# Kernel tuning notes

Measured on AMD Instinct MI355X. Metric: run time of the kernel, lower is better.

The kernel has to match this reference:

```python
import jax, jax.numpy as jnp
import numpy as np

N_NODES = 50000
N_EDGES = 640000
N_GRAPHS = 64
IN_DIM, HID, OUT_DIM = 128, 256, 4


def gcn_conv(x, src, dst, W, b, n_nodes):
    """PyG GCNConv: linear transform, then sym-normalized aggregation with self-loops."""
    h = x @ W  # [N, out]
    deg = jnp.zeros((n_nodes,), h.dtype).at[dst].add(1.0) + 1.0  # +1 self-loop
    dinv = jax.lax.rsqrt(deg)  # deg >= 1 always
    norm = dinv[src] * dinv[dst]  # [E]
    msg = h[src] * norm[:, None]  # [E, out]  gather + scale
    agg = jax.ops.segment_sum(msg, dst, num_segments=n_nodes)  # scatter-add
    agg = agg + h * (dinv * dinv)[:, None]  # self-loop contribution
    return agg + b


def global_mean_pool(x, batch, num_graphs):
    s = jax.ops.segment_sum(x, batch, num_segments=num_graphs)
    cnt = jax.ops.segment_sum(jnp.ones((x.shape[0],), x.dtype), batch, num_segments=num_graphs)
    return s / jnp.clip(cnt, 1.0)[:, None]


def setup_inputs() -> dict:
    key = jax.random.key(0)
    ks = jax.random.split(key, 8)
    x = jax.random.normal(ks[0], (N_NODES, IN_DIM), jnp.float32)
    src = jax.random.randint(ks[1], (N_EDGES,), 0, N_NODES, jnp.int64 if jax.config.jax_enable_x64 else jnp.int32)
    dst = jax.random.randint(ks[2], (N_EDGES,), 0, N_NODES, src.dtype)
    batch = jnp.sort(jax.random.randint(ks[3], (N_NODES,), 0, N_GRAPHS, src.dtype))
    W1 = jax.random.normal(ks[4], (IN_DIM, HID), jnp.float32) * (1.0 / np.sqrt(IN_DIM))
    b1 = jnp.zeros((HID,), jnp.float32)
    W2 = jax.random.normal(ks[5], (HID, HID // 2), jnp.float32) * (1.0 / np.sqrt(HID))
    b2 = jnp.zeros((HID // 2,), jnp.float32)
    Wfc = jax.random.normal(ks[6], (HID // 2, OUT_DIM), jnp.float32) * (1.0 / np.sqrt(HID // 2))
    bfc = jnp.zeros((OUT_DIM,), jnp.float32)
    return {"x": x, "src": src, "dst": dst, "batch": batch,
            "W1": W1, "b1": b1, "W2": W2, "b2": b2, "Wfc": Wfc, "bfc": bfc}


def reference(x, src, dst, batch, W1, b1, W2, b2, Wfc, bfc):
    n = x.shape[0]
    h = jax.nn.relu(gcn_conv(x, src, dst, W1, b1, n))   # dropout is identity at inference
    h = jax.nn.relu(gcn_conv(h, src, dst, W2, b2, n))
    g = global_mean_pool(h, batch, N_GRAPHS)            # [G, HID//2]
    return g @ Wfc + bfc                                # [G, OUT_DIM]
```

## Files before the change

### kernel.cpp

```cpp
#include <hip/hip_runtime.h>


constexpr int IN_DIM  = 128;
constexpr int HID     = 256;
constexpr int HID2    = 128;
constexpr int OUT_DIM = 4;
constexpr int NGRAPH  = 64;

typedef __attribute__((ext_vector_type(8))) short bf16x8;
typedef __attribute__((ext_vector_type(4))) float f32x4;

__device__ __forceinline__ short f2bf(float f) {
    union { float f; unsigned u; } v; v.f = f;
    unsigned r = v.u + 0x7fff + ((v.u >> 16) & 1);
    return (short)(r >> 16);
}
__device__ __forceinline__ float bf2f(short s) {
    union { unsigned u; float f; } v; v.u = ((unsigned)(unsigned short)s) << 16;
    return v.f;
}


__global__ void wprep_all_kernel(const float* __restrict__ W1, short* __restrict__ W1th,
                                 short* __restrict__ W1tl,
                                 const float* __restrict__ W2, short* __restrict__ W2th,
                                 short* __restrict__ W2tl,
                                 int* __restrict__ count, float* __restrict__ pool, int N) {
    int i = blockIdx.x * blockDim.x + threadIdx.x;
    if (i < IN_DIM * HID) {
        int k = i / HID, n = i % HID;
        float w = W1[i];
        short h = f2bf(w);
        W1th[n * IN_DIM + k] = h;
        W1tl[n * IN_DIM + k] = f2bf(w - bf2f(h));
    }
    if (i < HID * HID2) {
        int k = i / HID2, n = i % HID2;
        float w = W2[i];
        short h = f2bf(w);
        W2th[n * HID + k] = h;
        W2tl[n * HID + k] = f2bf(w - bf2f(h));
    }
    if (i < N) count[i] = 0;
    if (i < NGRAPH * HID2) pool[i] = 0.f;
}


__global__ void hist_kernel(const int* __restrict__ dst, int* __restrict__ count,
                            ushort* __restrict__ rank, int E) {
    int i = blockIdx.x * blockDim.x + threadIdx.x;
    if (i < E) rank[i] = (ushort)atomicAdd(&count[dst[i]], 1);
}

__global__ void scan1_kernel(const int* __restrict__ count, int* __restrict__ bsums, int N) {
    __shared__ int s[256];
    int t = threadIdx.x, i = blockIdx.x * 256 + t;
    int v = (i < N) ? count[i] : 0;
    s[t] = v; __syncthreads();
    for (int o = 1; o < 256; o <<= 1) {
        int x = (t >= o) ? s[t - o] : 0;
        __syncthreads(); s[t] += x; __syncthreads();
    }
    if (t == 255) bsums[blockIdx.x] = s[255];
}

__global__ void scan3_kernel(const int* __restrict__ count, const int* __restrict__ bsums,
                             int* __restrict__ rowptr, float* __restrict__ dinv,
                             int N, int E, int nb) {
    __shared__ int sb[256];
    __shared__ int s[256];
    int t = threadIdx.x, i = blockIdx.x * 256 + t;
    int bv = (t < nb) ? bsums[t] : 0;
    sb[t] = bv; __syncthreads();
    for (int o = 1; o < 256; o <<= 1) {
        int x = (t >= o) ? sb[t - o] : 0;
        __syncthreads(); sb[t] += x; __syncthreads();
    }
    int myex = (blockIdx.x == 0) ? 0 : sb[blockIdx.x - 1];
    int v = (i < N) ? count[i] : 0;
    s[t] = v; __syncthreads();
    for (int o = 1; o < 256; o <<= 1) {
        int x = (t >= o) ? s[t - o] : 0;
        __syncthreads(); s[t] += x; __syncthreads();
    }
    if (i < N) {
        rowptr[i] = myex + s[t] - v;
        dinv[i] = rsqrtf((float)v + 1.0f);
        if (i == 0) rowptr[N] = E;
    }
}

__global__ void scatter_scale_kernel(const int* __restrict__ src, const int* __restrict__ dst,
                                     const ushort* __restrict__ rank,
                                     const int* __restrict__ rowptr, ushort* __restrict__ csr,
                                     const float* __restrict__ x, const float* __restrict__ dinv,
                                     ushort* __restrict__ xb, int E, int total2) {
    int i = blockIdx.x * blockDim.x + threadIdx.x;
    if (i < E) {
        int p = rowptr[dst[i]] + (int)rank[i];
        csr[p] = (ushort)src[i];
    }
    if (i < total2) {
        float d = dinv[i >> 6];
        float2 v = ((const float2*)x)[i];
        ushort2 o;
        o.x = (ushort)f2bf(v.x * d);
        o.y = (ushort)f2bf(v.y * d);
        ((ushort2*)xb)[i] = o;
    }
}


__launch_bounds__(256, 2)
__global__ void mlp_fused_kernel(const short* __restrict__ A,
                                 const short* __restrict__ W1h, const short* __restrict__ W1l,
                                 const float* __restrict__ b1,
                                 const short* __restrict__ W2h, const short* __restrict__ W2l,
                                 const float* __restrict__ dinv,
                                 short* __restrict__ Cb, int M) {
    __shared__ __align__(16) short L[12288 + 6144];
    short* A1 = L;
    short* A0 = L + 12288;
    __shared__ float dinv_s[48];

    const int tid  = threadIdx.x;
    const int w    = tid >> 6;
    const int lane = tid & 63;
    const int l15  = lane & 15;
    const int kq8  = (lane >> 4) * 8;
    const int row0 = blockIdx.x * 48;

    const short* w1hp = W1h + (size_t)(w * 64 + l15) * IN_DIM + kq8;
    const short* w1lp = W1l + (size_t)(w * 64 + l15) * IN_DIM + kq8;
    bf16x8 wh1[4][4], wl1[4][4];
#pragma unroll
    for (int ks = 0; ks < 4; ++ks)
#pragma unroll
        for (int n = 0; n < 4; ++n) {
            wh1[ks][n] = *(const bf16x8*)(w1hp + (size_t)(n * 16) * IN_DIM + ks * 32);
            wl1[ks][n] = *(const bf16x8*)(w1lp + (size_t)(n * 16) * IN_DIM + ks * 32);
        }

    {
        bf16x8 stg[3];
#pragma unroll
        for (int j = 0; j < 3; ++j) {
            int s = w * 3 + j;
            int m = s >> 2, ks = s & 3;
            int rr = row0 + m * 16 + l15; if (rr >= M) rr = M - 1;
            stg[j] = *(const bf16x8*)(A + (size_t)rr * IN_DIM + ks * 32 + kq8);
        }
#pragma unroll
        for (int j = 0; j < 3; ++j)
            *(bf16x8*)&A0[(w * 3 + j) * 512 + lane * 8] = stg[j];
    }
    if (tid < 48) { int r = row0 + tid; dinv_s[tid] = dinv[r < M ? r : M - 1]; }
    __syncthreads();

    f32x4 acc1[3][4];
#pragma unroll
    for (int m = 0; m < 3; ++m)
#pragma unroll
        for (int n = 0; n < 4; ++n) acc1[m][n] = f32x4{0.f, 0.f, 0.f, 0.f};

#pragma unroll
    for (int ks = 0; ks < 4; ++ks) {
        bf16x8 af[3];
#pragma unroll
        for (int m = 0; m < 3; ++m) af[m] = *(const bf16x8*)&A0[(m * 4 + ks) * 512 + lane * 8];
#pragma unroll
        for (int m = 0; m < 3; ++m)
#pragma unroll
            for (int n = 0; n < 4; ++n) {
                acc1[m][n] = __builtin_amdgcn_mfma_f32_16x16x32_bf16(af[m], wh1[ks][n], acc1[m][n], 0, 0, 0);
                acc1[m][n] = __builtin_amdgcn_mfma_f32_16x16x32_bf16(af[m], wl1[ks][n], acc1[m][n], 0, 0, 0);
            }
    }

#pragma unroll
    for (int n = 0; n < 4; ++n) {
        int c  = w * 64 + n * 16 + l15;
        float bv = b1[c];
        int kst = c >> 5;
        int q  = (c >> 3) & 3;
        int e  = c & 7;
#pragma unroll
        for (int m = 0; m < 3; ++m)
#pragma unroll
            for (int r4 = 0; r4 < 4; ++r4) {
                int rl = (lane >> 4) * 4 + r4;
                int d  = rl + 16 * q;
                float v = fmaxf(acc1[m][n][r4] + bv, 0.f);
                A1[(m * 8 + kst) * 512 + d * 8 + e] = f2bf(v);
            }
    }

    const short* w2hp = W2h + (size_t)(w * 32 + l15) * HID + kq8;
    const short* w2lp = W2l + (size_t)(w * 32 + l15) * HID + kq8;
    bf16x8 wh2[8][2], wl2[8][2];
#pragma unroll
    for (int ks = 0; ks < 8; ++ks)
#pragma unroll
        for (int n = 0; n < 2; ++n) {
            wh2[ks][n] = *(const bf16x8*)(w2hp + (size_t)(n * 16) * HID + ks * 32);
            wl2[ks][n] = *(const bf16x8*)(w2lp + (size_t)(n * 16) * HID + ks * 32);
        }
    __syncthreads();

    f32x4 acc2[3][2];
#pragma unroll
    for (int m = 0; m < 3; ++m)
#pragma unroll
        for (int n = 0; n < 2; ++n) acc2[m][n] = f32x4{0.f, 0.f, 0.f, 0.f};

#pragma unroll
    for (int ks = 0; ks < 8; ++ks) {
        bf16x8 af[3];
#pragma unroll
        for (int m = 0; m < 3; ++m) af[m] = *(const bf16x8*)&A1[(m * 8 + ks) * 512 + lane * 8];
#pragma unroll
        for (int m = 0; m < 3; ++m)
#pragma unroll
            for (int n = 0; n < 2; ++n) {
                acc2[m][n] = __builtin_amdgcn_mfma_f32_16x16x32_bf16(af[m], wh2[ks][n], acc2[m][n], 0, 0, 0);
                acc2[m][n] = __builtin_amdgcn_mfma_f32_16x16x32_bf16(af[m], wl2[ks][n], acc2[m][n], 0, 0, 0);
            }
    }
    __syncthreads();

    short* T = A1;
#pragma unroll
    for (int n = 0; n < 2; ++n) {
        int c = w * 32 + n * 16 + l15;
#pragma unroll
        for (int m = 0; m < 3; ++m)
#pragma unroll
            for (int r4 = 0; r4 < 4; ++r4) {
                int r = m * 16 + (lane >> 4) * 4 + r4;
                T[r * 132 + c] = f2bf(acc2[m][n][r4] * dinv_s[r]);
            }
    }
    __syncthreads();
#pragma unroll
    for (int it = 0; it < 3; ++it) {
        int chunk = it * 256 + tid;
        int lr = chunk >> 4;
        int lc = (chunk & 15) * 8;
        int gr = row0 + lr;
        if (gr < M)
            *(bf16x8*)(Cb + (size_t)gr * HID2 + lc) = *(const bf16x8*)&T[lr * 132 + lc];
    }
}


template <bool POOL>
__launch_bounds__(256)
__global__ void agg_group_kernel(const ushort* __restrict__ hb, const float* __restrict__ dinv,
                                 const int* __restrict__ rowptr, const ushort* __restrict__ csr,
                                 const float* __restrict__ bias,
                                 short* __restrict__ oh,
                                 const int* __restrict__ batch, float* __restrict__ pool,
                                 int N) {
    __shared__ float pacc[16][128];
    __shared__ int   sgid[16];

    const int tid  = threadIdx.x;
    const int li   = tid & 15;
    const int nib  = tid >> 4;
    const int node = blockIdx.x * 16 + nib;
    const bool valid = node < N;
    if (!POOL && !valid) return;
    const int cw = valid ? node : N - 1;

    const int lo = rowptr[cw], hi = rowptr[cw + 1];
    const float dd = dinv[cw];

    float a[8];
    {
        bf16x8 sv = *(const bf16x8*)(hb + ((size_t)cw << 7) + (li << 3));
#pragma unroll
        for (int d = 0; d < 8; ++d) a[d] = bf2f(sv[d]);
    }

    const ushort* hsl = hb + (li << 3);

    for (int base = lo; base < hi; base += 16) {
        int cnt = min(16, hi - base);
        int sidx = (int)csr[base + (li < cnt ? li : cnt - 1)];
        bf16x8 p[8], q[8];
#pragma unroll
        for (int u = 0; u < 8; ++u) {
            int s = __shfl(sidx, u < cnt ? u : cnt - 1, 16);
            p[u] = *(const bf16x8*)(hsl + ((size_t)s << 7));
        }
#pragma unroll
        for (int u = 0; u < 8; ++u) {
            int e = 8 + u;
            int s = __shfl(sidx, e < cnt ? e : cnt - 1, 16);
            q[u] = *(const bf16x8*)(hsl + ((size_t)s << 7));
        }
#pragma unroll
        for (int u = 0; u < 8; ++u) {
            bool v = u < cnt;
#pragma unroll
            for (int d = 0; d < 8; ++d) a[d] += v ? bf2f(p[u][d]) : 0.f;
        }
#pragma unroll
        for (int u = 0; u < 8; ++u) {
            bool v = 8 + u < cnt;
#pragma unroll
            for (int d = 0; d < 8; ++d) a[d] += v ? bf2f(q[u][d]) : 0.f;
        }
    }

#pragma unroll
    for (int d = 0; d < 8; ++d) a[d] *= dd;

    if (!POOL) {
        if (valid) {
            bf16x8 o;
#pragma unroll
            for (int d = 0; d < 8; ++d) o[d] = f2bf(a[d]);
            *(bf16x8*)&oh[(size_t)node * 128 + li * 8] = o;
        }
        return;
    }

    {
        float4 b0 = ((const float4*)bias)[li * 2];
        float4 b1 = ((const float4*)bias)[li * 2 + 1];
        a[0] = fmaxf(a[0] + b0.x, 0.f); a[1] = fmaxf(a[1] + b0.y, 0.f);
        a[2] = fmaxf(a[2] + b0.z, 0.f); a[3] = fmaxf(a[3] + b0.w, 0.f);
        a[4] = fmaxf(a[4] + b1.x, 0.f); a[5] = fmaxf(a[5] + b1.y, 0.f);
        a[6] = fmaxf(a[6] + b1.z, 0.f); a[7] = fmaxf(a[7] + b1.w, 0.f);
    }
    if (li == 0) sgid[nib] = valid ? batch[node] : -1;
#pragma unroll
    for (int d = 0; d < 8; ++d) pacc[nib][li * 8 + d] = a[d];
    __syncthreads();
    if (tid < 128) {
        int c = tid;
        int cur = sgid[0];
        float run = 0.f;
#pragma unroll 1
        for (int w = 0; w < 16; ++w) {
            int gi = sgid[w];
            if (gi < 0) break;
            if (gi != cur) { atomicAdd(&pool[cur * HID2 + c], run); run = 0.f; cur = gi; }
            run += pacc[w][c];
        }
        atomicAdd(&pool[cur * HID2 + c], run);
    }
}


__device__ __forceinline__ int lower_bound_i(const int* __restrict__ a, int n, int key) {
    int lo = 0, hi = n;
    while (lo < hi) {
        int mid = (lo + hi) >> 1;
        if (a[mid] < key) lo = mid + 1; else hi = mid;
    }
    return lo;
}

__global__ void fc_kernel(const float* __restrict__ pool, const int* __restrict__ batch,
                          const float* __restrict__ Wfc, const float* __restrict__ bfc,
                          float* __restrict__ out, int N) {
    int t = threadIdx.x;
    int g = t >> 2, o = t & 3;
    int lo = lower_bound_i(batch, N, g);
    int hi = lower_bound_i(batch, N, g + 1);
    float acc = 0.f;
#pragma unroll 8
    for (int c = 0; c < HID2; ++c)
        acc = fmaf(pool[g * HID2 + c], Wfc[c * OUT_DIM + o], acc);
    float inv = 1.0f / fmaxf((float)(hi - lo), 1.0f);
    out[g * OUT_DIM + o] = acc * inv + bfc[o];
}

extern "C" void kernel_launch(void* const* d_in, const int* in_sizes, int n_in,
                              void* d_out, int out_size, void* d_ws, size_t ws_size,
                              hipStream_t stream) {
    const float* x   = (const float*)d_in[0];
    const int* src   = (const int*)d_in[1];
    const int* dst   = (const int*)d_in[2];
    const int* batch = (const int*)d_in[3];
    const float* W1  = (const float*)d_in[4];
    const float* b1  = (const float*)d_in[5];
    const float* W2  = (const float*)d_in[6];
    const float* b2  = (const float*)d_in[7];
    const float* Wfc = (const float*)d_in[8];
    const float* bfc = (const float*)d_in[9];
    float* out = (float*)d_out;

    const int N = in_sizes[0] / IN_DIM;
    const int E = in_sizes[1];
    const int NB = (N + 255) / 256;
    const int GA = (N + 15) / 16;
    const int GM = (N + 47) / 48;

    char* ws = (char*)d_ws;
    size_t off = 0;
    auto alloc = [&](size_t bytes) {
        char* p = ws + off;
        off = (off + bytes + 255) & ~(size_t)255;
        return p;
    };
    float*  dinv   = (float*) alloc((size_t)N * 4);
    int*    count  = (int*)   alloc((size_t)N * 4);
    int*    rowptr = (int*)   alloc((size_t)(N + 1) * 4);
    int*    bsums  = (int*)   alloc(256 * 4);
    ushort* rank   = (ushort*)alloc((size_t)E * 2);
    ushort* csr    = (ushort*)alloc((size_t)E * 2);
    short*  W1th   = (short*) alloc((size_t)IN_DIM * HID * 2);
    short*  W1tl   = (short*) alloc((size_t)IN_DIM * HID * 2);
    short*  W2th   = (short*) alloc((size_t)HID * HID2 * 2);
    short*  W2tl   = (short*) alloc((size_t)HID * HID2 * 2);
    ushort* xb     = (ushort*)alloc((size_t)N * IN_DIM * 2);
    short*  axb    = (short*) alloc((size_t)N * IN_DIM * 2);
    float*  pool   = (float*) alloc((size_t)NGRAPH * HID2 * 4);
    ushort* h2b = xb;

    wprep_all_kernel<<<(max(IN_DIM * HID, N) + 255) / 256, 256, 0, stream>>>(
        W1, W1th, W1tl, W2, W2th, W2tl, count, pool, N);

    hist_kernel<<<(E + 255) / 256, 256, 0, stream>>>(dst, count, rank, E);
    scan1_kernel<<<NB, 256, 0, stream>>>(count, bsums, N);
    scan3_kernel<<<NB, 256, 0, stream>>>(count, bsums, rowptr, dinv, N, E, NB);
    scatter_scale_kernel<<<(N * 64 + 255) / 256, 256, 0, stream>>>(
        src, dst, rank, rowptr, csr, x, dinv, xb, E, N * 64);

    agg_group_kernel<false><<<GA, 256, 0, stream>>>(
        xb, dinv, rowptr, csr, nullptr, axb, nullptr, nullptr, N);

    mlp_fused_kernel<<<GM, 256, 0, stream>>>(
        axb, W1th, W1tl, b1, W2th, W2tl, dinv, (short*)h2b, N);

    agg_group_kernel<true><<<GA, 256, 0, stream>>>(
        h2b, dinv, rowptr, csr, b2, nullptr, batch, pool, N);

    fc_kernel<<<1, NGRAPH * OUT_DIM, 0, stream>>>(pool, batch, Wfc, bfc, out, N);
}
```

Baseline: 248.9 us.

## Pre-swizzle weights into MFMA fragment layout and process two row tiles per block

The weight-prep kernel now writes W1/W2 hi/lo bf16 splits directly in per-lane MFMA fragment order, so the fused MLP kernel loads each fragment with contiguous coalesced 16-byte reads instead of strided transposed rows. The MLP kernel also loops over two 48-row tiles per block, reusing the register-resident W1 fragments and halving the grid. This amortizes weight loads across more rows. The cost is fewer blocks to fill the GPU, an extra barrier per tile, and W2 fragments reloaded inside the loop.

```diff
diff --git a/kernel.cpp b/kernel.cpp
--- a/kernel.cpp
+++ b/kernel.cpp
@@ -21,25 +21,31 @@
 }
 
 
-__global__ void wprep_all_kernel(const float* __restrict__ W1, short* __restrict__ W1th,
-                                 short* __restrict__ W1tl,
-                                 const float* __restrict__ W2, short* __restrict__ W2th,
-                                 short* __restrict__ W2tl,
+__global__ void wprep_all_kernel(const float* __restrict__ W1, short* __restrict__ W1fh,
+                                 short* __restrict__ W1fl,
+                                 const float* __restrict__ W2, short* __restrict__ W2fh,
+                                 short* __restrict__ W2fl,
                                  int* __restrict__ count, float* __restrict__ pool, int N) {
     int i = blockIdx.x * blockDim.x + threadIdx.x;
     if (i < IN_DIM * HID) {
-        int k = i / HID, n = i % HID;
-        float w = W1[i];
+        int slab = i >> 9, lane = (i >> 3) & 63, e = i & 7;
+        int c4 = slab >> 2, ks = slab & 3;
+        int col = c4 * 16 + (lane & 15);
+        int k   = ks * 32 + (lane >> 4) * 8 + e;
+        float w = W1[k * HID + col];
         short h = f2bf(w);
-        W1th[n * IN_DIM + k] = h;
-        W1tl[n * IN_DIM + k] = f2bf(w - bf2f(h));
+        W1fh[i] = h;
+        W1fl[i] = f2bf(w - bf2f(h));
     }
     if (i < HID * HID2) {
-        int k = i / HID2, n = i % HID2;
-        float w = W2[i];
+        int slab = i >> 9, lane = (i >> 3) & 63, e = i & 7;
+        int c4 = slab >> 3, ks = slab & 7;
+        int col = c4 * 16 + (lane & 15);
+        int k   = ks * 32 + (lane >> 4) * 8 + e;
+        float w = W2[k * HID2 + col];
         short h = f2bf(w);
-        W2th[n * HID + k] = h;
-        W2tl[n * HID + k] = f2bf(w - bf2f(h));
+        W2fh[i] = h;
+        W2fl[i] = f2bf(w - bf2f(h));
     }
     if (i < N) count[i] = 0;
     if (i < NGRAPH * HID2) pool[i] = 0.f;
@@ -128,127 +134,130 @@
     const int lane = tid & 63;
     const int l15  = lane & 15;
     const int kq8  = (lane >> 4) * 8;
-    const int row0 = blockIdx.x * 48;
-
-    const short* w1hp = W1h + (size_t)(w * 64 + l15) * IN_DIM + kq8;
-    const short* w1lp = W1l + (size_t)(w * 64 + l15) * IN_DIM + kq8;
+
     bf16x8 wh1[4][4], wl1[4][4];
 #pragma unroll
     for (int ks = 0; ks < 4; ++ks)
 #pragma unroll
         for (int n = 0; n < 4; ++n) {
-            wh1[ks][n] = *(const bf16x8*)(w1hp + (size_t)(n * 16) * IN_DIM + ks * 32);
-            wl1[ks][n] = *(const bf16x8*)(w1lp + (size_t)(n * 16) * IN_DIM + ks * 32);
-        }
-
-    {
-        bf16x8 stg[3];
-#pragma unroll
-        for (int j = 0; j < 3; ++j) {
-            int s = w * 3 + j;
-            int m = s >> 2, ks = s & 3;
-            int rr = row0 + m * 16 + l15; if (rr >= M) rr = M - 1;
-            stg[j] = *(const bf16x8*)(A + (size_t)rr * IN_DIM + ks * 32 + kq8);
-        }
-#pragma unroll
-        for (int j = 0; j < 3; ++j)
-            *(bf16x8*)&A0[(w * 3 + j) * 512 + lane * 8] = stg[j];
-    }
-    if (tid < 48) { int r = row0 + tid; dinv_s[tid] = dinv[r < M ? r : M - 1]; }
-    __syncthreads();
-
-    f32x4 acc1[3][4];
-#pragma unroll
-    for (int m = 0; m < 3; ++m)
-#pragma unroll
-        for (int n = 0; n < 4; ++n) acc1[m][n] = f32x4{0.f, 0.f, 0.f, 0.f};
-
-#pragma unroll
-    for (int ks = 0; ks < 4; ++ks) {
-        bf16x8 af[3];
-#pragma unroll
-        for (int m = 0; m < 3; ++m) af[m] = *(const bf16x8*)&A0[(m * 4 + ks) * 512 + lane * 8];
+            int slab = ((w * 4 + n) * 4 + ks) * 512;
+            wh1[ks][n] = *(const bf16x8*)(W1h + slab + lane * 8);
+            wl1[ks][n] = *(const bf16x8*)(W1l + slab + lane * 8);
+        }
+
+#pragma unroll 1
+    for (int t = 0; t < 2; ++t) {
+        const int row0 = (blockIdx.x * 2 + t) * 48;
+
+        {
+            bf16x8 stg[3];
+#pragma unroll
+            for (int j = 0; j < 3; ++j) {
+                int s = w * 3 + j;
+                int m = s >> 2, ks = s & 3;
+                int rr = row0 + m * 16 + l15; if (rr >= M) rr = M - 1;
+                stg[j] = *(const bf16x8*)(A + (size_t)rr * IN_DIM + ks * 32 + kq8);
+            }
+#pragma unroll
+            for (int j = 0; j < 3; ++j)
+                *(bf16x8*)&A0[(w * 3 + j) * 512 + lane * 8] = stg[j];
+        }
+        if (tid < 48) { int r = row0 + tid; dinv_s[tid] = dinv[r < M ? r : M - 1]; }
+        __syncthreads();
+
+        f32x4 acc1[3][4];
 #pragma unroll
         for (int m = 0; m < 3; ++m)
 #pragma unroll
-            for (int n = 0; n < 4; ++n) {
-                acc1[m][n] = __builtin_amdgcn_mfma_f32_16x16x32_bf16(af[m], wh1[ks][n], acc1[m][n], 0, 0, 0);
-                acc1[m][n] = __builtin_amdgcn_mfma_f32_16x16x32_bf16(af[m], wl1[ks][n], acc1[m][n], 0, 0, 0);
+            for (int n = 0; n < 4; ++n) acc1[m][n] = f32x4{0.f, 0.f, 0.f, 0.f};
+
+#pragma unroll
+        for (int ks = 0; ks < 4; ++ks) {
+            bf16x8 af[3];
+#pragma unroll
+            for (int m = 0; m < 3; ++m) af[m] = *(const bf16x8*)&A0[(m * 4 + ks) * 512 + lane * 8];
+#pragma unroll
+            for (int m = 0; m < 3; ++m)
+#pragma unroll
+                for (int n = 0; n < 4; ++n) {
+                    acc1[m][n] = __builtin_amdgcn_mfma_f32_16x16x32_bf16(af[m], wh1[ks][n], acc1[m][n], 0, 0, 0);
+                    acc1[m][n] = __builtin_amdgcn_mfma_f32_16x16x32_bf16(af[m], wl1[ks][n], acc1[m][n], 0, 0, 0);
+                }
+        }
+
+#pragma unroll
+        for (int n = 0; n < 4; ++n) {
+            int c  = w * 64 + n * 16 + l15;
+            float bv = b1[c];
+            int kst = c >> 5;
+            int q  = (c >> 3) & 3;
+            int e  = c & 7;
+#pragma unroll
+            for (int m = 0; m < 3; ++m)
+#pragma unroll
+                for (int r4 = 0; r4 < 4; ++r4) {
+                    int rl = (lane >> 4) * 4 + r4;
+                    int d  = rl + 16 * q;
+                    float v = fmaxf(acc1[m][n][r4] + bv, 0.f);
+                    A1[(m * 8 + kst) * 512 + d * 8 + e] = f2bf(v);
+                }
+        }
+
+        bf16x8 wh2[8][2], wl2[8][2];
+#pragma unroll
+        for (int ks = 0; ks < 8; ++ks)
+#pragma unroll
+            for (int n = 0; n < 2; ++n) {
+                int slab = ((w * 2 + n) * 8 + ks) * 512;
+                wh2[ks][n] = *(const bf16x8*)(W2h + slab + lane * 8);
+                wl2[ks][n] = *(const bf16x8*)(W2l + slab + lane * 8);
             }
-    }
-
-#pragma unroll
-    for (int n = 0; n < 4; ++n) {
-        int c  = w * 64 + n * 16 + l15;
-        float bv = b1[c];
-        int kst = c >> 5;
-        int q  = (c >> 3) & 3;
-        int e  = c & 7;
+        __syncthreads();
+
+        f32x4 acc2[3][2];
 #pragma unroll
         for (int m = 0; m < 3; ++m)
 #pragma unroll
-            for (int r4 = 0; r4 < 4; ++r4) {
-                int rl = (lane >> 4) * 4 + r4;
-                int d  = rl + 16 * q;
-                float v = fmaxf(acc1[m][n][r4] + bv, 0.f);
-                A1[(m * 8 + kst) * 512 + d * 8 + e] = f2bf(v);
-            }
-    }
-
-    const short* w2hp = W2h + (size_t)(w * 32 + l15) * HID + kq8;
-    const short* w2lp = W2l + (size_t)(w * 32 + l15) * HID + kq8;
-    bf16x8 wh2[8][2], wl2[8][2];
-#pragma unroll
-    for (int ks = 0; ks < 8; ++ks)
+            for (int n = 0; n < 2; ++n) acc2[m][n] = f32x4{0.f, 0.f, 0.f, 0.f};
+
+#pragma unroll
+        for (int ks = 0; ks < 8; ++ks) {
+            bf16x8 af[3];
+#pragma unroll
+            for (int m = 0; m < 3; ++m) af[m] = *(const bf16x8*)&A1[(m * 8 + ks) * 512 + lane * 8];
+#pragma unroll
+            for (int m = 0; m < 3; ++m)
+#pragma unroll
+                for (int n = 0; n < 2; ++n) {
+                    acc2[m][n] = __builtin_amdgcn_mfma_f32_16x16x32_bf16(af[m], wh2[ks][n], acc2[m][n], 0, 0, 0);
+                    acc2[m][n] = __builtin_amdgcn_mfma_f32_16x16x32_bf16(af[m], wl2[ks][n], acc2[m][n], 0, 0, 0);
+                }
+        }
+        __syncthreads();
+
+        short* T = A1;
 #pragma unroll
         for (int n = 0; n < 2; ++n) {
-            wh2[ks][n] = *(const bf16x8*)(w2hp + (size_t)(n * 16) * HID + ks * 32);
-            wl2[ks][n] = *(const bf16x8*)(w2lp + (size_t)(n * 16) * HID + ks * 32);
-        }
-    __syncthreads();
-
-    f32x4 acc2[3][2];
-#pragma unroll
-    for (int m = 0; m < 3; ++m)
-#pragma unroll
-        for (int n = 0; n < 2; ++n) acc2[m][n] = f32x4{0.f, 0.f, 0.f, 0.f};
-
-#pragma unroll
-    for (int ks = 0; ks < 8; ++ks) {
-        bf16x8 af[3];
-#pragma unroll
-        for (int m = 0; m < 3; ++m) af[m] = *(const bf16x8*)&A1[(m * 8 + ks) * 512 + lane * 8];
-#pragma unroll
-        for (int m = 0; m < 3; ++m)
-#pragma unroll
-            for (int n = 0; n < 2; ++n) {
-                acc2[m][n] = __builtin_amdgcn_mfma_f32_16x16x32_bf16(af[m], wh2[ks][n], acc2[m][n], 0, 0, 0);
-                acc2[m][n] = __builtin_amdgcn_mfma_f32_16x16x32_bf16(af[m], wl2[ks][n], acc2[m][n], 0, 0, 0);
-            }
-    }
-    __syncthreads();
-
-    short* T = A1;
-#pragma unroll
-    for (int n = 0; n < 2; ++n) {
-        int c = w * 32 + n * 16 + l15;
-#pragma unroll
-        for (int m = 0; m < 3; ++m)
-#pragma unroll
-            for (int r4 = 0; r4 < 4; ++r4) {
-                int r = m * 16 + (lane >> 4) * 4 + r4;
-                T[r * 132 + c] = f2bf(acc2[m][n][r4] * dinv_s[r]);
-            }
-    }
-    __syncthreads();
-#pragma unroll
-    for (int it = 0; it < 3; ++it) {
-        int chunk = it * 256 + tid;
-        int lr = chunk >> 4;
-        int lc = (chunk & 15) * 8;
-        int gr = row0 + lr;
-        if (gr < M)
-            *(bf16x8*)(Cb + (size_t)gr * HID2 + lc) = *(const bf16x8*)&T[lr * 132 + lc];
+            int c = w * 32 + n * 16 + l15;
+#pragma unroll
+            for (int m = 0; m < 3; ++m)
+#pragma unroll
+                for (int r4 = 0; r4 < 4; ++r4) {
+                    int r = m * 16 + (lane >> 4) * 4 + r4;
+                    T[r * 132 + c] = f2bf(acc2[m][n][r4] * dinv_s[r]);
+                }
+        }
+        __syncthreads();
+#pragma unroll
+        for (int it = 0; it < 3; ++it) {
+            int chunk = it * 256 + tid;
+            int lr = chunk >> 4;
+            int lc = (chunk & 15) * 8;
+            int gr = row0 + lr;
+            if (gr < M)
+                *(bf16x8*)(Cb + (size_t)gr * HID2 + lc) = *(const bf16x8*)&T[lr * 132 + lc];
+        }
+        __syncthreads();
     }
 }
 
@@ -397,7 +406,7 @@
     const int E = in_sizes[1];
     const int NB = (N + 255) / 256;
     const int GA = (N + 15) / 16;
-    const int GM = (N + 47) / 48;
+    const int GM = (N + 95) / 96;
 
     char* ws = (char*)d_ws;
     size_t off = 0;
```

Result: slower. 269.0 us (+8.1%).
